# Optimization experiments

Hardware: AMD Instinct MI355X
Metric: run time of the kernel (lower is better)

Reference implementation:

```python
import jax, jax.numpy as jnp
import numpy as np

PATCH = 4
WINDOW = 4
MAX_ROUNDS = 4
MIN_ROUNDS = 2
LAMBDA_P = 0.2
TOPK = 8


def _ln(x, g, b, eps=1e-5):
    m = x.mean(-1, keepdims=True)
    v = ((x - m) ** 2).mean(-1, keepdims=True)
    return (x - m) / jnp.sqrt(v + eps) * g + b


def _mlp(x, w1, b1, w2, b2):
    # Linear -> exact GELU -> Linear (matches nn.GELU default)
    return jax.nn.gelu(x @ w1 + b1, approximate=False) @ w2 + b2


def setup_inputs() -> dict:
    key = jax.random.key(0)
    ks = jax.random.split(key, 24)
    B, T, D, V = 16, 4096, 256, 256
    s = 0.02
    w = lambda i, shape: jax.random.normal(ks[i], shape, jnp.float32) * s
    z = lambda *shape: jnp.zeros(shape, jnp.float32)
    o = lambda *shape: jnp.ones(shape, jnp.float32)
    return {
        'x': jax.random.randint(ks[0], (B, T), 0, V),
        'emb': w(1, (V, D)), 'pos': w(2, (PATCH, D)),
        'gru_wih': w(3, (D, 3 * D)), 'gru_whh': w(4, (D, 3 * D)),
        'gru_bih': z(3 * D), 'gru_bhh': z(3 * D),
        'ln_p_g': o(D), 'ln_p_b': z(D),
        'sum_w': w(5, (D, D)), 'sum_b': z(D),
        'msg_w1': w(6, (2 * D, D)), 'msg_b1': z(D), 'msg_w2': w(7, (D, D)), 'msg_b2': z(D),
        'upd_w1': w(8, (2 * D, D)), 'upd_b1': z(D), 'upd_w2': w(9, (D, D)), 'upd_b2': z(D),
        'halt_w': w(10, (D, 1)), 'halt_b': z(1),
        'ln_mp_g': o(D), 'ln_mp_b': z(D),
        'q_w': w(11, (D, D)), 'q_b': z(D),
        'k_w': w(12, (D, D)), 'k_b': z(D),
        'v_w': w(13, (D, D)), 'v_b': z(D),
        'o_w': w(14, (D, D)), 'o_b': z(D),
        'bc_w': w(15, (D, D)), 'bc_b': z(D),
        'ln_f_g': o(D), 'ln_f_b': z(D),
        'head_w': w(16, (D, V)),
    }


def reference(x, emb, pos, gru_wih, gru_whh, gru_bih, gru_bhh, ln_p_g, ln_p_b,
              sum_w, sum_b, msg_w1, msg_b1, msg_w2, msg_b2, upd_w1, upd_b1,
              upd_w2, upd_b2, halt_w, halt_b, ln_mp_g, ln_mp_b, q_w, q_b,
              k_w, k_b, v_w, v_b, o_w, o_b, bc_w, bc_b, ln_f_g, ln_f_b, head_w):
    B, T = x.shape
    D = emb.shape[1]
    Np = T // PATCH  # T is divisible by PATCH for these shapes (no pad needed)

    # --- GRU patch processor over B*Np sequences of length PATCH ---
    tok = x.reshape(B * Np, PATCH)
    hseq = emb[tok] + pos[None]  # [BN, P, D]

    def gru_step(h, xt):
        gi = xt @ gru_wih + gru_bih
        gh = h @ gru_whh + gru_bhh
        ir, iz, inn = jnp.split(gi, 3, -1)
        hr, hz, hn = jnp.split(gh, 3, -1)
        r = jax.nn.sigmoid(ir + hr)
        zz = jax.nn.sigmoid(iz + hz)
        n = jnp.tanh(inn + r * hn)
        h = (1 - zz) * n + zz * h
        return h, h

    h0 = jnp.zeros((B * Np, D), hseq.dtype)
    _, gout = jax.lax.scan(gru_step, h0, jnp.swapaxes(hseq, 0, 1))
    local = _ln(jnp.swapaxes(gout, 0, 1), ln_p_g, ln_p_b).reshape(B, Np, PATCH, D)
    summaries = local.mean(2) @ sum_w + sum_b  # [B, Np, D]

    # --- Local message passing with ACT-style halting (fixed MAX_ROUNDS) ---
    h = summaries
    remaining = jnp.ones((B, Np, 1), h.dtype)
    out_mp = jnp.zeros_like(h)
    kl = jnp.zeros((), h.dtype)
    for step in range(MAX_ROUNDS):
        padded = jnp.pad(h, ((0, 0), (WINDOW, 0), (0, 0)))
        # neighbors: self plus previous WINDOW patches -> [B, Np, W+1, D]
        neigh = jnp.stack([padded[:, WINDOW - w:WINDOW - w + Np] for w in range(WINDOW + 1)], axis=2)
        self_exp = jnp.broadcast_to(h[:, :, None, :], neigh.shape)
        msgs = _mlp(jnp.concatenate([self_exp, neigh], -1), msg_w1, msg_b1, msg_w2, msg_b2).mean(2)
        h = _ln(h + _mlp(jnp.concatenate([h, msgs], -1), upd_w1, upd_b1, upd_w2, upd_b2), ln_mp_g, ln_mp_b)
        if step < MIN_ROUNDS:
            hp = jnp.zeros((B, Np, 1), h.dtype)
        else:
            hp = jax.nn.sigmoid(h.mean(1, keepdims=True) @ halt_w + halt_b)  # [B,1,1]
            hp = jnp.broadcast_to(hp, (B, Np, 1))
        if step == MAX_ROUNDS - 1:
            hp = jnp.ones_like(hp)
        out_mp = out_mp + remaining * hp * h
        remaining = remaining * (1 - hp)
        p_geom = LAMBDA_P * (1 - LAMBDA_P) ** step
        # F.kl_div(log(mean+eps), log(p_geom), log_target=True) = p*(log p - log(mean+eps))
        kl = kl + p_geom * (np.log(p_geom) - jnp.log(hp.mean() + 1e-8))
    kl = kl / MAX_ROUNDS

    # --- Sparse top-k causal retrieval ---
    q = out_mp @ q_w + q_b
    kk = out_mp @ k_w + k_b
    v = out_mp @ v_w + v_b
    scores = jnp.einsum('bnd,bmd->bnm', q, kk) / np.sqrt(D).astype(np.float32)
    causal = jnp.tril(jnp.ones((Np, Np), bool))
    neg = jnp.asarray(-jnp.inf, scores.dtype)
    scores = jnp.where(causal[None], scores, neg)
    vals, idx = jax.lax.top_k(scores, TOPK)  # [B, Np, k]
    bi = jnp.arange(B)[:, None, None]
    ni = jnp.arange(Np)[None, :, None]
    sparse = jnp.full_like(scores, neg).at[bi, ni, idx].set(vals)
    attn = jax.nn.softmax(sparse, axis=-1)
    retrieved = jnp.einsum('bnm,bmd->bnd', attn, v) @ o_w + o_b

    # --- Broadcast back to tokens and project ---
    combined = out_mp + retrieved
    broad = combined @ bc_w + bc_b
    final = (local + broad[:, :, None, :]).reshape(B, Np * PATCH, D)[:, :T]
    logits = _ln(final, ln_f_g, ln_f_b) @ head_w
    return logits, kl
```

## Files before the change

### kernel.cpp

```cpp
#include <hip/hip_runtime.h>
#include <math.h>


typedef __bf16 bf16_t;
typedef bf16_t bf16x8 __attribute__((ext_vector_type(8)));
typedef bf16_t bf16x4 __attribute__((ext_vector_type(4)));
typedef float f32x4 __attribute__((ext_vector_type(4)));

#define GF_BIAS 1
#define GF_GELU 4
#define GF_RES 8
#define GF_SCAUSAL 16
#define GF_F32OUT 32

__device__ __forceinline__ float gelu_exact(float x) {
  return 0.5f * x * (1.0f + erff(x * 0.7071067811865475f));
}

__device__ __forceinline__ float sigm(float x) { return 1.f / (1.f + expf(-x)); }

__device__ __forceinline__ float wave_sum(float v) {
#pragma unroll
  for (int o = 32; o; o >>= 1) v += __shfl_xor(v, o, 64);
  return v;
}

__device__ __forceinline__ void gload16(const void* g, void* l) {
  __builtin_amdgcn_global_load_lds(
      (const __attribute__((address_space(1))) void*)g,
      (__attribute__((address_space(3))) void*)l, 16, 0, 0);
}

__device__ __forceinline__ unsigned long long skey(float s, int m) {
  unsigned u = __float_as_uint(s);
  u ^= (u & 0x80000000u) ? 0xFFFFFFFFu : 0x80000000u;
  return ((unsigned long long)u << 32) | (unsigned)(0x7FFFFFFF - m);
}

template<int FLAGS>
__global__ __launch_bounds__(256)
void gemm_bt(const bf16_t* __restrict__ A, const bf16_t* __restrict__ Bt,
             void* __restrict__ Cv, const float* __restrict__ bias,
             const bf16_t* __restrict__ res,
             int lda, int ldb, int ldc, int ldr,
             long long sA, long long sB, long long sC, float scale)
{
  __shared__ __align__(16) bf16_t As[128][64];
  __shared__ __align__(16) bf16_t Bs[128][64];
  const int z = blockIdx.z;
  A  += (long long)z * sA;
  Bt += (long long)z * sB;
  const int m0 = blockIdx.x * 128, n0 = blockIdx.y * 128;
  if ((FLAGS & GF_SCAUSAL) && n0 > m0) return;
  const int tid = threadIdx.x, lane = tid & 63, wave = tid >> 6;
  const int wm = (wave >> 1) << 6, wn = (wave & 1) << 6;
  const int lr = lane & 15, lg = lane >> 4;
  const int cx = lane & 7;

  const int srow = wave * 32 + (lane >> 3);
  const int scol = (((lane & 7) ^ ((lane >> 3) & 7)) * 8);
  const bf16_t* ga = A  + (long long)(m0 + srow) * lda + scol;
  const bf16_t* gb = Bt + (long long)(n0 + srow) * ldb + scol;
  char* lA = (char*)(&As[srow][0]) + (lane & 7) * 16;
  char* lB = (char*)(&Bs[srow][0]) + (lane & 7) * 16;

  f32x4 acc[4][4] = {};

#pragma unroll
  for (int kt = 0; kt < 4; kt++) {
    const int ko = kt * 64;
#pragma unroll
    for (int q = 0; q < 4; q++) {
      gload16(ga + (long long)q * 8 * lda + ko, lA + q * 1024);
      gload16(gb + (long long)q * 8 * ldb + ko, lB + q * 1024);
    }
    __syncthreads();
#pragma unroll
    for (int kk = 0; kk < 2; kk++) {
      const int co = ((kk * 4 + lg) ^ cx) << 4;
      bf16x8 af[4], bfv[4];
#pragma unroll
      for (int i = 0; i < 4; i++)
        af[i]  = *(const bf16x8*)((char*)As + (wm + i * 16 + lr) * 128 + co);
#pragma unroll
      for (int j = 0; j < 4; j++)
        bfv[j] = *(const bf16x8*)((char*)Bs + (wn + j * 16 + lr) * 128 + co);
#pragma unroll
      for (int i = 0; i < 4; i++)
#pragma unroll
        for (int j = 0; j < 4; j++)
          acc[i][j] = __builtin_amdgcn_mfma_f32_16x16x32_bf16(af[i], bfv[j], acc[i][j], 0, 0, 0);
    }
    if (kt < 3) __syncthreads();
  }

#pragma unroll
  for (int i = 0; i < 4; i++) {
#pragma unroll
    for (int j = 0; j < 4; j++) {
      const int col = n0 + wn + j * 16 + lr;
      const float bval = (FLAGS & GF_BIAS) ? bias[col] : 0.f;
#pragma unroll
      for (int e = 0; e < 4; e++) {
        const int row = m0 + wm + i * 16 + lg * 4 + e;
        float v = acc[i][j][e];
        if (FLAGS & GF_SCAUSAL) { v *= scale; if (col > row) v = -__builtin_inff(); }
        v += bval;
        if (FLAGS & GF_RES) v += (float)res[(long long)row * ldr + col];
        if (FLAGS & GF_GELU) v = gelu_exact(v);
        const long long ci = (long long)z * sC + (long long)row * ldc + col;
        if (FLAGS & GF_F32OUT) ((float*)Cv)[ci] = v;
        else                   ((bf16_t*)Cv)[ci] = (bf16_t)v;
      }
    }
  }
}

template<int FLAGS>
__global__ __launch_bounds__(256)
void gemm64(const bf16_t* __restrict__ A, const bf16_t* __restrict__ Bt,
            void* __restrict__ Cv, const float* __restrict__ bias,
            const bf16_t* __restrict__ res,
            int lda, int ldb, int ldc, int ldr)
{
  __shared__ __align__(16) bf16_t As[64][64];
  __shared__ __align__(16) bf16_t Bs[64][64];
  const int m0 = blockIdx.x * 64, n0 = blockIdx.y * 64;
  const int tid = threadIdx.x, lane = tid & 63, wave = tid >> 6;
  const int wm = (wave >> 1) * 32, wn = (wave & 1) * 32;
  const int lr = lane & 15, lg = lane >> 4;
  const int cx = lane & 7;

  const int srow = tid >> 3;
  const int scol = (((tid & 7) ^ (srow & 7)) * 8);
  const bf16_t* ga = A  + (long long)(m0 + srow) * lda + scol;
  const bf16_t* gb = Bt + (long long)(n0 + srow) * ldb + scol;
  char* lA = (char*)As + tid * 16;
  char* lB = (char*)Bs + tid * 16;

  f32x4 acc[2][2] = {};

#pragma unroll
  for (int kt = 0; kt < 4; kt++) {
    const int ko = kt * 64;
    gload16(ga + ko, lA);
    gload16(ga + 32LL * lda + ko, lA + 4096);
    gload16(gb + ko, lB);
    gload16(gb + 32LL * ldb + ko, lB + 4096);
    __syncthreads();
#pragma unroll
    for (int kk = 0; kk < 2; kk++) {
      const int co = ((kk * 4 + lg) ^ cx) << 4;
      bf16x8 af[2], bfv[2];
#pragma unroll
      for (int i = 0; i < 2; i++)
        af[i]  = *(const bf16x8*)((char*)As + (wm + i * 16 + lr) * 128 + co);
#pragma unroll
      for (int j = 0; j < 2; j++)
        bfv[j] = *(const bf16x8*)((char*)Bs + (wn + j * 16 + lr) * 128 + co);
#pragma unroll
      for (int i = 0; i < 2; i++)
#pragma unroll
        for (int j = 0; j < 2; j++)
          acc[i][j] = __builtin_amdgcn_mfma_f32_16x16x32_bf16(af[i], bfv[j], acc[i][j], 0, 0, 0);
    }
    if (kt < 3) __syncthreads();
  }

#pragma unroll
  for (int i = 0; i < 2; i++) {
#pragma unroll
    for (int j = 0; j < 2; j++) {
      const int col = n0 + wn + j * 16 + lr;
      const float bval = (FLAGS & GF_BIAS) ? bias[col] : 0.f;
#pragma unroll
      for (int e = 0; e < 4; e++) {
        const int row = m0 + wm + i * 16 + lg * 4 + e;
        float v = acc[i][j][e] + bval;
        if (FLAGS & GF_RES) v += (float)res[(long long)row * ldr + col];
        if (FLAGS & GF_GELU) v = gelu_exact(v);
        const long long ci = (long long)row * ldc + col;
        if (FLAGS & GF_F32OUT) ((float*)Cv)[ci] = v;
        else                   ((bf16_t*)Cv)[ci] = (bf16_t)v;
      }
    }
  }
}

struct TD { const float* src; bf16_t* dst; int N; int k0; int ld; };
struct PrepArgs {
  TD d[16];
  const float* emb; const float* pos; bf16_t* XE;
  const float* msg_b1; const float* msg_b2; const float* upd_w1; const float* upd_b1;
  const float* q_b; const float* k_b; const float* v_b;
  float* BIAS3; float* QKVB;
};

__global__ __launch_bounds__(256) void k_prep(PrepArgs pa) {
  const int y = blockIdx.y, x = blockIdx.x, d = threadIdx.x;
  if (y < 16) {
    TD t = pa.d[y];
    if (x >= t.N) return;
    if (t.k0 < 0) t.dst[(long long)x * 256 + d] = (bf16_t)t.src[(long long)x * t.ld + d];
    else          t.dst[(long long)x * 256 + d] = (bf16_t)t.src[(long long)(t.k0 + d) * t.ld + x];
  } else if (y == 16) {
    const int p = x >> 8, v = x & 255;
    pa.XE[(long long)x * 256 + d] = (bf16_t)(pa.emb[v * 256 + d] + pa.pos[p * 256 + d]);
  } else {
    if      (x == 0) pa.BIAS3[d] = pa.msg_b1[d];
    else if (x == 1) pa.BIAS3[256 + d] = 0.f;
    else if (x == 2) {
      float acc = pa.upd_b1[d];
      for (int k = 0; k < 256; k++) acc += pa.msg_b2[k] * pa.upd_w1[(long long)(256 + k) * 256 + d];
      pa.BIAS3[512 + d] = acc;
    }
    else if (x == 3) pa.QKVB[d] = pa.q_b[d];
    else if (x == 4) pa.QKVB[256 + d] = pa.k_b[d];
    else if (x == 5) pa.QKVB[512 + d] = pa.v_b[d];
  }
}

__global__ __launch_bounds__(64)
void k_gru_gate(const int* __restrict__ x, const bf16_t* __restrict__ gitab,
                const bf16_t* __restrict__ GH, const float* __restrict__ bhh,
                bf16_t* __restrict__ H, bf16_t* __restrict__ LOC, int t)
{
  const int s = blockIdx.x, lane = threadIdx.x, d0 = lane * 4;
  const int v = x[s * 4 + t];
  const bf16_t* gi = gitab + (long long)(t * 256 + v) * 768;
  const bf16x4 g_r = *(const bf16x4*)(gi + d0);
  const bf16x4 g_z = *(const bf16x4*)(gi + 256 + d0);
  const bf16x4 g_n = *(const bf16x4*)(gi + 512 + d0);
  float hr[4], hz[4], hn[4], hp[4];
  if (t == 0) {
#pragma unroll
    for (int e = 0; e < 4; e++) {
      hr[e] = bhh[d0 + e]; hz[e] = bhh[256 + d0 + e]; hn[e] = bhh[512 + d0 + e];
      hp[e] = 0.f;
    }
  } else {
    const bf16_t* gh = GH + (long long)s * 768;
    const bf16x4 a = *(const bf16x4*)(gh + d0);
    const bf16x4 b4 = *(const bf16x4*)(gh + 256 + d0);
    const bf16x4 c4 = *(const bf16x4*)(gh + 512 + d0);
    const bf16x4 hv = *(const bf16x4*)(H + (long long)s * 256 + d0);
#pragma unroll
    for (int e = 0; e < 4; e++) { hr[e] = a[e]; hz[e] = b4[e]; hn[e] = c4[e]; hp[e] = hv[e]; }
  }
  bf16x4 ho;
#pragma unroll
  for (int e = 0; e < 4; e++) {
    const float r = sigm((float)g_r[e] + hr[e]);
    const float zz = sigm((float)g_z[e] + hz[e]);
    const float nn = tanhf((float)g_n[e] + r * hn[e]);
    ho[e] = (bf16_t)((1.f - zz) * nn + zz * hp[e]);
  }
  *(bf16x4*)(H + (long long)s * 256 + d0) = ho;
  *(bf16x4*)(LOC + ((long long)s * 4 + t) * 256 + d0) = ho;
}

__global__ __launch_bounds__(64)
void k_ln(const bf16_t* __restrict__ X, const bf16_t* __restrict__ ADD, int addmode,
          bf16_t* __restrict__ OUT, const float* __restrict__ g,
          const float* __restrict__ b)
{
  const long long r = blockIdx.x;
  const int d0 = threadIdx.x * 4;
  const bf16x4 xv = *(const bf16x4*)(X + r * 256 + d0);
  float xf[4];
#pragma unroll
  for (int e = 0; e < 4; e++) xf[e] = (float)xv[e];
  if (addmode == 1) {
    const bf16x4 av = *(const bf16x4*)(ADD + r * 256 + d0);
#pragma unroll
    for (int e = 0; e < 4; e++) xf[e] += (float)av[e];
  } else if (addmode == 2) {
    const bf16x4 av = *(const bf16x4*)(ADD + (r >> 2) * 256 + d0);
#pragma unroll
    for (int e = 0; e < 4; e++) xf[e] += (float)av[e];
  }
  const float mean = wave_sum(xf[0] + xf[1] + xf[2] + xf[3]) * (1.f / 256.f);
  float q = 0.f;
#pragma unroll
  for (int e = 0; e < 4; e++) { const float dx = xf[e] - mean; q += dx * dx; }
  const float rstd = rsqrtf(wave_sum(q) * (1.f / 256.f) + 1e-5f);
  const float4 gv = *(const float4*)(g + d0);
  const float4 bv = *(const float4*)(b + d0);
  const float gg[4] = {gv.x, gv.y, gv.z, gv.w};
  const float bb[4] = {bv.x, bv.y, bv.z, bv.w};
  bf16x4 ov;
#pragma unroll
  for (int e = 0; e < 4; e++) ov[e] = (bf16_t)((xf[e] - mean) * rstd * gg[e] + bb[e]);
  *(bf16x4*)(OUT + r * 256 + d0) = ov;
}

__global__ __launch_bounds__(64)
void k_lnp4(bf16_t* __restrict__ LOC, bf16_t* __restrict__ SUMB,
            const float* __restrict__ g, const float* __restrict__ b)
{
  const long long s = blockIdx.x;
  const int d0 = threadIdx.x * 4;
  const float4 gv = *(const float4*)(g + d0);
  const float4 bv = *(const float4*)(b + d0);
  const float gg[4] = {gv.x, gv.y, gv.z, gv.w};
  const float bb[4] = {bv.x, bv.y, bv.z, bv.w};
  float accd[4] = {0.f, 0.f, 0.f, 0.f};
#pragma unroll
  for (int t = 0; t < 4; t++) {
    bf16_t* row = LOC + (s * 4 + t) * 256 + d0;
    const bf16x4 xv = *(const bf16x4*)row;
    float xf[4];
#pragma unroll
    for (int e = 0; e < 4; e++) xf[e] = (float)xv[e];
    const float mean = wave_sum(xf[0] + xf[1] + xf[2] + xf[3]) * (1.f / 256.f);
    float q = 0.f;
#pragma unroll
    for (int e = 0; e < 4; e++) { const float dx = xf[e] - mean; q += dx * dx; }
    const float rstd = rsqrtf(wave_sum(q) * (1.f / 256.f) + 1e-5f);
    bf16x4 ov;
#pragma unroll
    for (int e = 0; e < 4; e++) {
      const float y = (xf[e] - mean) * rstd * gg[e] + bb[e];
      ov[e] = (bf16_t)y;
      accd[e] += y;
    }
    *(bf16x4*)row = ov;
  }
  bf16x4 sv;
#pragma unroll
  for (int e = 0; e < 4; e++) sv[e] = (bf16_t)(accd[e] * 0.25f);
  *(bf16x4*)(SUMB + s * 256 + d0) = sv;
}

__global__ __launch_bounds__(64)
void k_gelumix(const bf16_t* __restrict__ A3, bf16_t* __restrict__ G)
{
  const long long s = blockIdx.x;
  const int n = (int)(s & 1023);
  const int d0 = threadIdx.x * 4;
  const bf16x4 av = *(const bf16x4*)(A3 + s * 768 + d0);
  float a[4];
#pragma unroll
  for (int e = 0; e < 4; e++) a[e] = (float)av[e];
  float acc[4] = {0.f, 0.f, 0.f, 0.f};
  const bf16_t* bbase = A3 + s * 768 + 256 + d0;
#pragma unroll
  for (int w = 0; w <= 4; w++) {
    if (n >= w) {
      const bf16x4 bn = *(const bf16x4*)(bbase - (long long)w * 768);
#pragma unroll
      for (int e = 0; e < 4; e++) acc[e] += gelu_exact(a[e] + (float)bn[e]);
    } else {
#pragma unroll
      for (int e = 0; e < 4; e++) acc[e] += gelu_exact(a[e]);
    }
  }
  bf16x4 ov;
#pragma unroll
  for (int e = 0; e < 4; e++) ov[e] = (bf16_t)(acc[e] * 0.2f);
  *(bf16x4*)(G + s * 256 + d0) = ov;
}

__global__ __launch_bounds__(64)
void k_halt1(const bf16_t* __restrict__ Hm, float* __restrict__ PS) {
  const int c = blockIdx.x, b = blockIdx.y, d0 = threadIdx.x * 4;
  float acc[4] = {0.f, 0.f, 0.f, 0.f};
  const bf16_t* base = Hm + ((long long)b * 1024 + c * 32) * 256 + d0;
#pragma unroll 4
  for (int n = 0; n < 32; n++) {
    const bf16x4 hv = *(const bf16x4*)(base + (long long)n * 256);
#pragma unroll
    for (int e = 0; e < 4; e++) acc[e] += (float)hv[e];
  }
  float4 o4; o4.x = acc[0]; o4.y = acc[1]; o4.z = acc[2]; o4.w = acc[3];
  *(float4*)(PS + ((long long)b * 32 + c) * 256 + d0) = o4;
}

__global__ __launch_bounds__(64)
void k_halt2(const float* __restrict__ PS, const float* __restrict__ hw,
             const float* __restrict__ hb, float* __restrict__ HP) {
  const int b = blockIdx.x, d0 = threadIdx.x * 4;
  float acc[4] = {0.f, 0.f, 0.f, 0.f};
  for (int c = 0; c < 32; c++) {
    const float4 p4 = *(const float4*)(PS + ((long long)b * 32 + c) * 256 + d0);
    acc[0] += p4.x; acc[1] += p4.y; acc[2] += p4.z; acc[3] += p4.w;
  }
  const float4 w4 = *(const float4*)(hw + d0);
  float val = (acc[0] * w4.x + acc[1] * w4.y + acc[2] * w4.z + acc[3] * w4.w) * (1.f / 1024.f);
  val = wave_sum(val);
  if (threadIdx.x == 0) HP[b] = sigm(val + hb[0]);
}

__global__ void k_kl(const float* __restrict__ HP, float* __restrict__ out) {
  float s = 0.f;
  for (int b = 0; b < 16; b++) s += HP[b];
  const float hpm = s * (1.f / 16.f);
  const float l8 = logf(1e-8f);
  const float p0 = 0.2f, p1 = 0.16f, p2 = 0.128f, p3 = 0.1024f;
  const float kl = p0 * (logf(p0) - l8)
                 + p1 * (logf(p1) - l8)
                 + p2 * (logf(p2) - logf(hpm + 1e-8f))
                 + p3 * (logf(p3) - logf(1.f + 1e-8f));
  out[0] = kl * 0.25f;
}

__global__ __launch_bounds__(64)
void k_outmp(const bf16_t* __restrict__ Hm, const float* __restrict__ HP,
             bf16_t* __restrict__ O, int acc) {
  const long long s = blockIdx.x;
  const int d0 = threadIdx.x * 4;
  const int b = (int)(s >> 10);
  const float hp = HP[b];
  const bf16x4 hv = *(const bf16x4*)(Hm + s * 256 + d0);
  bf16x4 ov;
  if (acc) {
    const bf16x4 pv = *(const bf16x4*)(O + s * 256 + d0);
#pragma unroll
    for (int e = 0; e < 4; e++) ov[e] = (bf16_t)((float)pv[e] + (1.f - hp) * (float)hv[e]);
  } else {
#pragma unroll
    for (int e = 0; e < 4; e++) ov[e] = (bf16_t)(hp * (float)hv[e]);
  }
  *(bf16x4*)(O + s * 256 + d0) = ov;
}

__global__ __launch_bounds__(256)
void k_topk(const float* __restrict__ S, const bf16_t* __restrict__ QKV,
            bf16_t* __restrict__ O) {
  const int n = blockIdx.x * 4 + (threadIdx.x >> 6);
  const int b = blockIdx.y;
  const int lane = threadIdx.x & 63;
  const float* srow = S + ((long long)(b * 1024 + n)) * 1024;
  unsigned long long kv[8] = {0, 0, 0, 0, 0, 0, 0, 0};
  for (int mb = lane * 4; mb <= n; mb += 256) {
    const float4 s4 = *(const float4*)(srow + mb);
    const float sv[4] = {s4.x, s4.y, s4.z, s4.w};
#pragma unroll
    for (int jj = 0; jj < 4; jj++) {
      const int m = mb + jj;
      if (m <= n) {
        const unsigned long long k = skey(sv[jj], m);
        if (k > kv[7]) {
          kv[7] = k;
#pragma unroll
          for (int j = 7; j > 0; j--) {
            if (kv[j] > kv[j-1]) {
              const unsigned long long t = kv[j]; kv[j] = kv[j-1]; kv[j-1] = t;
            }
          }
        }
      }
    }
  }
  float wv[8]; int wi[8];
#pragma unroll
  for (int r = 0; r < 8; r++) {
    unsigned long long mk = kv[0];
#pragma unroll
    for (int off = 32; off; off >>= 1) {
      const unsigned long long ok = __shfl_xor(mk, off, 64);
      if (ok > mk) mk = ok;
    }
    if (mk != 0ull) {
      unsigned hi = (unsigned)(mk >> 32);
      hi ^= (hi & 0x80000000u) ? 0x80000000u : 0xFFFFFFFFu;
      wv[r] = __uint_as_float(hi);
      wi[r] = 0x7FFFFFFF - (int)(unsigned)(mk & 0xFFFFFFFFu);
    } else {
      wv[r] = 0.f; wi[r] = -1;
    }
    if (kv[0] == mk && mk != 0ull) {
#pragma unroll
      for (int j = 0; j < 7; j++) kv[j] = kv[j + 1];
      kv[7] = 0ull;
    }
  }
  const float mx = wv[0];
  float w[8]; float den = 0.f;
#pragma unroll
  for (int j = 0; j < 8; j++) {
    w[j] = (wi[j] >= 0) ? expf(wv[j] - mx) : 0.f;
    den += w[j];
  }
  const float inv = 1.f / den;
  float a[4] = {0.f, 0.f, 0.f, 0.f};
#pragma unroll
  for (int j = 0; j < 8; j++) {
    if (wi[j] >= 0) {
      const bf16x4 vv = *(const bf16x4*)(QKV + ((long long)b * 1024 + wi[j]) * 768 + 512 + lane * 4);
      const float wj = w[j] * inv;
#pragma unroll
      for (int e = 0; e < 4; e++) a[e] = fmaf(wj, (float)vv[e], a[e]);
    }
  }
  bf16x4 o4;
#pragma unroll
  for (int e = 0; e < 4; e++) o4[e] = (bf16_t)a[e];
  *(bf16x4*)(O + ((long long)(b * 1024 + n)) * 256 + lane * 4) = o4;
}

extern "C" void kernel_launch(void* const* d_in, const int* in_sizes, int n_in,
                              void* d_out, int out_size, void* d_ws, size_t ws_size,
                              hipStream_t stream) {
  (void)in_sizes; (void)n_in; (void)ws_size;
  const int*   x      = (const int*)d_in[0];
  const float* emb    = (const float*)d_in[1];
  const float* pos    = (const float*)d_in[2];
  const float* wih    = (const float*)d_in[3];
  const float* whh    = (const float*)d_in[4];
  const float* bih    = (const float*)d_in[5];
  const float* bhh    = (const float*)d_in[6];
  const float* lnp_g  = (const float*)d_in[7];
  const float* lnp_b  = (const float*)d_in[8];
  const float* sum_w  = (const float*)d_in[9];
  const float* sum_b  = (const float*)d_in[10];
  const float* msg_w1 = (const float*)d_in[11];
  const float* msg_b1 = (const float*)d_in[12];
  const float* msg_w2 = (const float*)d_in[13];
  const float* msg_b2 = (const float*)d_in[14];
  const float* upd_w1 = (const float*)d_in[15];
  const float* upd_b1 = (const float*)d_in[16];
  const float* upd_w2 = (const float*)d_in[17];
  const float* upd_b2 = (const float*)d_in[18];
  const float* halt_w = (const float*)d_in[19];
  const float* halt_b = (const float*)d_in[20];
  const float* lnm_g  = (const float*)d_in[21];
  const float* lnm_b  = (const float*)d_in[22];
  const float* q_b    = (const float*)d_in[24];
  const float* k_b    = (const float*)d_in[26];
  const float* v_b    = (const float*)d_in[28];
  const float* o_b    = (const float*)d_in[30];
  const float* bc_b   = (const float*)d_in[32];
  const float* lnf_g  = (const float*)d_in[33];
  const float* lnf_b  = (const float*)d_in[34];

  char* base = (char*)d_ws;
  size_t off = 0;
  auto alloc = [&](size_t bytes) -> void* {
    void* p = (void*)(base + off);
    off += (bytes + 255) & ~(size_t)255;
    return p;
  };
  const size_t SL2 = 16384ull * 256 * 2;
  bf16_t* WIHT  = (bf16_t*)alloc(768 * 256 * 2);
  bf16_t* WHHT  = (bf16_t*)alloc(768 * 256 * 2);
  bf16_t* SUMT  = (bf16_t*)alloc(256 * 256 * 2);
  bf16_t* MW    = (bf16_t*)alloc(768 * 256 * 2);
  bf16_t* W2T   = (bf16_t*)alloc(256 * 256 * 2);
  bf16_t* W2NT  = (bf16_t*)alloc(256 * 256 * 2);
  bf16_t* UW1MT = (bf16_t*)alloc(256 * 256 * 2);
  bf16_t* UW2T  = (bf16_t*)alloc(256 * 256 * 2);
  bf16_t* WCB   = (bf16_t*)alloc(256 * 256 * 2);
  bf16_t* QKVW  = (bf16_t*)alloc(768 * 256 * 2);
  bf16_t* OT    = (bf16_t*)alloc(256 * 256 * 2);
  bf16_t* BCT   = (bf16_t*)alloc(256 * 256 * 2);
  bf16_t* HEADT = (bf16_t*)alloc(256 * 256 * 2);
  float*  BIAS3 = (float*)alloc(768 * 4);
  float*  QKVB  = (float*)alloc(768 * 4);
  bf16_t* XE    = (bf16_t*)alloc(1024ull * 256 * 2);
  bf16_t* GITAB = (bf16_t*)alloc(1024ull * 768 * 2);
  bf16_t* LOCb  = (bf16_t*)alloc(65536ull * 256 * 2);

  char*   SCR   = (char*)alloc(16ull * 1024 * 1024 * 4);
  float*  SCORES = (float*)SCR;
  bf16_t* GH    = (bf16_t*)SCR;
  bf16_t* H     = (bf16_t*)(SCR + 25165824);
  bf16_t* SUMB  = (bf16_t*)(SCR + 33554432);
  bf16_t* A3    = (bf16_t*)(SCR + 41943040);

  bf16_t* HMP   = (bf16_t*)alloc(SL2);
  bf16_t* G     = (bf16_t*)alloc(SL2);
  bf16_t* BROAD = (bf16_t*)alloc(SL2);
  bf16_t* UB    = (bf16_t*)alloc(SL2);
  bf16_t* U2B   = (bf16_t*)alloc(SL2);
  bf16_t* OUTMP = (bf16_t*)alloc(SL2);
  bf16_t* QKV   = (bf16_t*)alloc(16384ull * 768 * 2);
  float*  PS    = (float*)alloc(512ull * 256 * 4);
  float*  HP    = (float*)alloc(64);
  bf16_t* ATT   = UB;
  bf16_t* COMB  = U2B;
  float*  out   = (float*)d_out;
  float*  klout = out + (out_size - 1);

  PrepArgs pa;
  pa.d[0]  = { wih,                    WIHT,            768, 0,   768 };
  pa.d[1]  = { whh,                    WHHT,            768, 0,   768 };
  pa.d[2]  = { sum_w,                  SUMT,            256, 0,   256 };
  pa.d[3]  = { msg_w1,                 MW,              256, 0,   256 };
  pa.d[4]  = { msg_w1,                 MW + 256 * 256,  256, 256, 256 };
  pa.d[5]  = { upd_w1,                 MW + 512 * 256,  256, 0,   256 };
  pa.d[6]  = { msg_w2,                 W2T,             256, 0,   256 };
  pa.d[7]  = { upd_w1,                 UW1MT,           256, 256, 256 };
  pa.d[8]  = { upd_w2,                 UW2T,            256, 0,   256 };
  pa.d[9]  = { (const float*)d_in[23], QKVW,            256, 0,   256 };
  pa.d[10] = { (const float*)d_in[25], QKVW + 256*256,  256, 0,   256 };
  pa.d[11] = { (const float*)d_in[27], QKVW + 512*256,  256, 0,   256 };
  pa.d[12] = { (const float*)d_in[29], OT,              256, 0,   256 };
  pa.d[13] = { (const float*)d_in[31], BCT,             256, 0,   256 };
  pa.d[14] = { (const float*)d_in[35], HEADT,           256, 0,   256 };
  pa.d[15] = { msg_w2,                 W2NT,            256, -1,  256 };
  pa.emb = emb; pa.pos = pos; pa.XE = XE;
  pa.msg_b1 = msg_b1; pa.msg_b2 = msg_b2; pa.upd_w1 = upd_w1; pa.upd_b1 = upd_b1;
  pa.q_b = q_b; pa.k_b = k_b; pa.v_b = v_b;
  pa.BIAS3 = BIAS3; pa.QKVB = QKVB;
  k_prep<<<dim3(1024, 18), 256, 0, stream>>>(pa);

  gemm64<0><<<dim3(4, 4), 256, 0, stream>>>(
      UW1MT, W2NT, WCB, nullptr, nullptr, 256, 256, 256, 0);

  gemm64<GF_BIAS><<<dim3(16, 12), 256, 0, stream>>>(
      XE, WIHT, GITAB, bih, nullptr, 256, 256, 768, 0);

  k_gru_gate<<<16384, 64, 0, stream>>>(x, GITAB, GH, bhh, H, LOCb, 0);
  for (int t = 1; t < 4; t++) {
    gemm64<GF_BIAS><<<dim3(256, 12), 256, 0, stream>>>(
        H, WHHT, GH, bhh, nullptr, 256, 256, 768, 0);
    k_gru_gate<<<16384, 64, 0, stream>>>(x, GITAB, GH, bhh, H, LOCb, t);
  }

  k_lnp4<<<16384, 64, 0, stream>>>(LOCb, SUMB, lnp_g, lnp_b);
  gemm64<GF_BIAS><<<dim3(256, 4), 256, 0, stream>>>(
      SUMB, SUMT, HMP, sum_b, nullptr, 256, 256, 256, 0);

  for (int step = 0; step < 4; step++) {
    gemm64<GF_BIAS><<<dim3(256, 12), 256, 0, stream>>>(
        HMP, MW, A3, BIAS3, nullptr, 256, 256, 768, 0);
    k_gelumix<<<16384, 64, 0, stream>>>(A3, G);
    gemm64<GF_RES | GF_GELU><<<dim3(256, 4), 256, 0, stream>>>(
        G, WCB, UB, nullptr, A3 + 512, 256, 256, 256, 768);
    gemm64<GF_BIAS><<<dim3(256, 4), 256, 0, stream>>>(
        UB, UW2T, U2B, upd_b2, nullptr, 256, 256, 256, 0);
    k_ln<<<16384, 64, 0, stream>>>(HMP, U2B, 1, HMP, lnm_g, lnm_b);
    if (step == 2) {
      k_halt1<<<dim3(32, 16), 64, 0, stream>>>(HMP, PS);
      k_halt2<<<16, 64, 0, stream>>>(PS, halt_w, halt_b, HP);
      k_kl<<<1, 1, 0, stream>>>(HP, klout);
      k_outmp<<<16384, 64, 0, stream>>>(HMP, HP, OUTMP, 0);
    } else if (step == 3) {
      k_outmp<<<16384, 64, 0, stream>>>(HMP, HP, OUTMP, 1);
    }
  }

  gemm64<GF_BIAS><<<dim3(256, 12), 256, 0, stream>>>(
      OUTMP, QKVW, QKV, QKVB, nullptr, 256, 256, 768, 0);
  gemm_bt<GF_SCAUSAL | GF_F32OUT><<<dim3(8, 8, 16), 256, 0, stream>>>(
      QKV, QKV + 256, SCORES, nullptr, nullptr, 768, 768, 1024, 0,
      1024LL * 768, 1024LL * 768, 1024LL * 1024, 0.0625f);
  k_topk<<<dim3(256, 16), 256, 0, stream>>>(SCORES, QKV, ATT);
  gemm64<GF_BIAS | GF_RES><<<dim3(256, 4), 256, 0, stream>>>(
      ATT, OT, COMB, o_b, OUTMP, 256, 256, 256, 256);
  gemm64<GF_BIAS><<<dim3(256, 4), 256, 0, stream>>>(
      COMB, BCT, BROAD, bc_b, nullptr, 256, 256, 256, 0);

  k_ln<<<65536, 64, 0, stream>>>(LOCb, BROAD, 2, LOCb, lnf_g, lnf_b);
  gemm_bt<GF_F32OUT><<<dim3(512, 2, 1), 256, 0, stream>>>(
      LOCb, HEADT, out, nullptr, nullptr, 256, 256, 256, 0, 0, 0, 0, 1.f);
}
```

Measured before the change: 491.6 us.

## Fuse causal score GEMM with top-k retrieval; use 128-tile GEMM for N=768

Replaces the batched causal score GEMM plus separate top-k kernel with a single kernel. Each wave computes 16 query rows' scores against key tiles using MFMA, keeps a running top-8 per row, then applies softmax and gathers V. This avoids writing and re-reading the 64 MB fp32 score matrix. It also switches the three 768-wide projection GEMMs from 64x64 tiles to the 128x128 gemm_bt kernel. The fused kernel launches only 1024 single-wave blocks with causal work imbalance, so it may be latency bound.

```diff
diff --git a/kernel.cpp b/kernel.cpp
--- a/kernel.cpp
+++ b/kernel.cpp
@@ -10,7 +10,6 @@
 #define GF_BIAS 1
 #define GF_GELU 4
 #define GF_RES 8
-#define GF_SCAUSAL 16
 #define GF_F32OUT 32
 
 __device__ __forceinline__ float gelu_exact(float x) {
@@ -42,16 +41,11 @@
 void gemm_bt(const bf16_t* __restrict__ A, const bf16_t* __restrict__ Bt,
              void* __restrict__ Cv, const float* __restrict__ bias,
              const bf16_t* __restrict__ res,
-             int lda, int ldb, int ldc, int ldr,
-             long long sA, long long sB, long long sC, float scale)
+             int lda, int ldb, int ldc, int ldr)
 {
   __shared__ __align__(16) bf16_t As[128][64];
   __shared__ __align__(16) bf16_t Bs[128][64];
-  const int z = blockIdx.z;
-  A  += (long long)z * sA;
-  Bt += (long long)z * sB;
   const int m0 = blockIdx.x * 128, n0 = blockIdx.y * 128;
-  if ((FLAGS & GF_SCAUSAL) && n0 > m0) return;
   const int tid = threadIdx.x, lane = tid & 63, wave = tid >> 6;
   const int wm = (wave >> 1) << 6, wn = (wave & 1) << 6;
   const int lr = lane & 15, lg = lane >> 4;
@@ -103,12 +97,10 @@
 #pragma unroll
       for (int e = 0; e < 4; e++) {
         const int row = m0 + wm + i * 16 + lg * 4 + e;
-        float v = acc[i][j][e];
-        if (FLAGS & GF_SCAUSAL) { v *= scale; if (col > row) v = -__builtin_inff(); }
-        v += bval;
+        float v = acc[i][j][e] + bval;
         if (FLAGS & GF_RES) v += (float)res[(long long)row * ldr + col];
         if (FLAGS & GF_GELU) v = gelu_exact(v);
-        const long long ci = (long long)z * sC + (long long)row * ldc + col;
+        const long long ci = (long long)row * ldc + col;
         if (FLAGS & GF_F32OUT) ((float*)Cv)[ci] = v;
         else                   ((bf16_t*)Cv)[ci] = (bf16_t)v;
       }
@@ -184,6 +176,135 @@
         else                   ((bf16_t*)Cv)[ci] = (bf16_t)v;
       }
     }
+  }
+}
+
+__global__ __launch_bounds__(64)
+void k_fatopk(const bf16_t* __restrict__ QKV, bf16_t* __restrict__ O) {
+  const int b = blockIdx.y;
+  const int qw = (int)((blockIdx.x + ((blockIdx.y * 21) & 63)) & 63);
+  const int lane = threadIdx.x;
+  const int lr = lane & 15, lg = lane >> 4;
+  const bf16_t* Qp = QKV + (long long)b * (1024LL * 768);
+  const bf16_t* Kp = Qp + 256;
+  const bf16_t* Vp = Qp + 512;
+  const int q0 = qw * 16;
+  const int qrow = q0 + lr;
+
+  bf16x8 bq[8];
+#pragma unroll
+  for (int s = 0; s < 8; s++)
+    bq[s] = *(const bf16x8*)(Qp + (long long)qrow * 768 + s * 32 + lg * 8);
+
+  unsigned long long kv[8] = {0ull, 0ull, 0ull, 0ull, 0ull, 0ull, 0ull, 0ull};
+
+#define INS8(KEY) {                                                     \
+    const unsigned long long k_ = (KEY);                                \
+    if (k_ > kv[7]) {                                                   \
+      kv[7] = k_;                                                       \
+      _Pragma("unroll")                                                 \
+      for (int j_ = 7; j_ > 0; j_--)                                    \
+        if (kv[j_] > kv[j_-1]) {                                        \
+          const unsigned long long t_ = kv[j_];                         \
+          kv[j_] = kv[j_-1]; kv[j_-1] = t_;                             \
+        }                                                               \
+    }                                                                   \
+  }
+
+  const int klim = qw + 1;
+  for (int kt = 0; kt < klim; kt += 2) {
+    const int kt2 = (kt + 1 < klim) ? kt + 1 : kt;
+    const bf16_t* ka = Kp + (long long)(kt  * 16 + lr) * 768 + lg * 8;
+    const bf16_t* kb = Kp + (long long)(kt2 * 16 + lr) * 768 + lg * 8;
+    bf16x8 afA[8], afB[8];
+#pragma unroll
+    for (int s = 0; s < 8; s++) afA[s] = *(const bf16x8*)(ka + s * 32);
+#pragma unroll
+    for (int s = 0; s < 8; s++) afB[s] = *(const bf16x8*)(kb + s * 32);
+    f32x4 a0 = {}, a1 = {};
+#pragma unroll
+    for (int s = 0; s < 8; s += 2) {
+      a0 = __builtin_amdgcn_mfma_f32_16x16x32_bf16(afA[s],     bq[s],     a0, 0, 0, 0);
+      a1 = __builtin_amdgcn_mfma_f32_16x16x32_bf16(afA[s + 1], bq[s + 1], a1, 0, 0, 0);
+    }
+#pragma unroll
+    for (int e = 0; e < 4; e++) {
+      const int m = kt * 16 + lg * 4 + e;
+      if (m <= qrow) INS8(skey((a0[e] + a1[e]) * 0.0625f, m));
+    }
+    if (kt2 != kt) {
+      f32x4 b0 = {}, b1 = {};
+#pragma unroll
+      for (int s = 0; s < 8; s += 2) {
+        b0 = __builtin_amdgcn_mfma_f32_16x16x32_bf16(afB[s],     bq[s],     b0, 0, 0, 0);
+        b1 = __builtin_amdgcn_mfma_f32_16x16x32_bf16(afB[s + 1], bq[s + 1], b1, 0, 0, 0);
+      }
+#pragma unroll
+      for (int e = 0; e < 4; e++) {
+        const int m = kt2 * 16 + lg * 4 + e;
+        if (m <= qrow) INS8(skey((b0[e] + b1[e]) * 0.0625f, m));
+      }
+    }
+  }
+#undef INS8
+
+  float wv[8]; int wi[8];
+#pragma unroll
+  for (int r = 0; r < 8; r++) {
+    unsigned long long mk = kv[0];
+    unsigned long long ok = __shfl_xor(mk, 16, 64); if (ok > mk) mk = ok;
+    ok = __shfl_xor(mk, 32, 64); if (ok > mk) mk = ok;
+    if (mk != 0ull) {
+      unsigned hi = (unsigned)(mk >> 32);
+      hi ^= (hi & 0x80000000u) ? 0x80000000u : 0xFFFFFFFFu;
+      wv[r] = __uint_as_float(hi);
+      wi[r] = 0x7FFFFFFF - (int)(unsigned)(mk & 0xFFFFFFFFu);
+    } else {
+      wv[r] = 0.f; wi[r] = -1;
+    }
+    if (kv[0] == mk && mk != 0ull) {
+#pragma unroll
+      for (int j = 0; j < 7; j++) kv[j] = kv[j + 1];
+      kv[7] = 0ull;
+    }
+  }
+
+  const float mx = wv[0];
+  float w8[8]; float den = 0.f;
+#pragma unroll
+  for (int j = 0; j < 8; j++) {
+    w8[j] = (wi[j] >= 0) ? expf(wv[j] - mx) : 0.f;
+    den += w8[j];
+  }
+  const float inv = 1.f / den;
+
+  f32x4 av[16] = {};
+#pragma unroll
+  for (int j = 0; j < 8; j++) {
+    if (wi[j] >= 0) {
+      const float wj = w8[j] * inv;
+      const bf16_t* vr = Vp + (long long)wi[j] * 768 + lg * 64;
+#pragma unroll
+      for (int c = 0; c < 8; c++) {
+        const bf16x8 vv = *(const bf16x8*)(vr + c * 8);
+#pragma unroll
+        for (int e = 0; e < 4; e++) {
+          av[2 * c][e]     = fmaf(wj, (float)vv[e],     av[2 * c][e]);
+          av[2 * c + 1][e] = fmaf(wj, (float)vv[4 + e], av[2 * c + 1][e]);
+        }
+      }
+    }
+  }
+  bf16_t* op = O + ((long long)b * 1024 + qrow) * 256 + lg * 64;
+#pragma unroll
+  for (int c = 0; c < 8; c++) {
+    bf16x8 ov;
+#pragma unroll
+    for (int e = 0; e < 4; e++) {
+      ov[e]     = (bf16_t)av[2 * c][e];
+      ov[4 + e] = (bf16_t)av[2 * c + 1][e];
+    }
+    *(bf16x8*)(op + c * 8) = ov;
   }
 }
 
@@ -422,81 +543,6 @@
     for (int e = 0; e < 4; e++) ov[e] = (bf16_t)(hp * (float)hv[e]);
   }
   *(bf16x4*)(O + s * 256 + d0) = ov;
-}
-
-__global__ __launch_bounds__(256)
-void k_topk(const float* __restrict__ S, const bf16_t* __restrict__ QKV,
-            bf16_t* __restrict__ O) {
-  const int n = blockIdx.x * 4 + (threadIdx.x >> 6);
-  const int b = blockIdx.y;
-  const int lane = threadIdx.x & 63;
-  const float* srow = S + ((long long)(b * 1024 + n)) * 1024;
-  unsigned long long kv[8] = {0, 0, 0, 0, 0, 0, 0, 0};
-  for (int mb = lane * 4; mb <= n; mb += 256) {
-    const float4 s4 = *(const float4*)(srow + mb);
-    const float sv[4] = {s4.x, s4.y, s4.z, s4.w};
-#pragma unroll
-    for (int jj = 0; jj < 4; jj++) {
-      const int m = mb + jj;
-      if (m <= n) {
-        const unsigned long long k = skey(sv[jj], m);
-        if (k > kv[7]) {
-          kv[7] = k;
-#pragma unroll
-          for (int j = 7; j > 0; j--) {
-            if (kv[j] > kv[j-1]) {
-              const unsigned long long t = kv[j]; kv[j] = kv[j-1]; kv[j-1] = t;
-            }
-          }
-        }
-      }
-    }
-  }
-  float wv[8]; int wi[8];
-#pragma unroll
-  for (int r = 0; r < 8; r++) {
-    unsigned long long mk = kv[0];
-#pragma unroll
-    for (int off = 32; off; off >>= 1) {
-      const unsigned long long ok = __shfl_xor(mk, off, 64);
-      if (ok > mk) mk = ok;
-    }
-    if (mk != 0ull) {
-      unsigned hi = (unsigned)(mk >> 32);
-      hi ^= (hi & 0x80000000u) ? 0x80000000u : 0xFFFFFFFFu;
-      wv[r] = __uint_as_float(hi);
-      wi[r] = 0x7FFFFFFF - (int)(unsigned)(mk & 0xFFFFFFFFu);
-    } else {
-      wv[r] = 0.f; wi[r] = -1;
-    }
-    if (kv[0] == mk && mk != 0ull) {
-#pragma unroll
-      for (int j = 0; j < 7; j++) kv[j] = kv[j + 1];
-      kv[7] = 0ull;
-    }
-  }
-  const float mx = wv[0];
-  float w[8]; float den = 0.f;
-#pragma unroll
-  for (int j = 0; j < 8; j++) {
-    w[j] = (wi[j] >= 0) ? expf(wv[j] - mx) : 0.f;
-    den += w[j];
-  }
-  const float inv = 1.f / den;
-  float a[4] = {0.f, 0.f, 0.f, 0.f};
-#pragma unroll
-  for (int j = 0; j < 8; j++) {
-    if (wi[j] >= 0) {
-      const bf16x4 vv = *(const bf16x4*)(QKV + ((long long)b * 1024 + wi[j]) * 768 + 512 + lane * 4);
-      const float wj = w[j] * inv;
-#pragma unroll
-      for (int e = 0; e < 4; e++) a[e] = fmaf(wj, (float)vv[e], a[e]);
-    }
-  }
-  bf16x4 o4;
-#pragma unroll
-  for (int e = 0; e < 4; e++) o4[e] = (bf16_t)a[e];
-  *(bf16x4*)(O + ((long long)(b * 1024 + n)) * 256 + lane * 4) = o4;
 }
 
 extern "C" void kernel_launch(void* const* d_in, const int* in_sizes, int n_in,
@@ -562,7 +608,6 @@
   bf16_t* LOCb  = (bf16_t*)alloc(65536ull * 256 * 2);
 
   char*   SCR   = (char*)alloc(16ull * 1024 * 1024 * 4);
-  float*  SCORES = (float*)SCR;
   bf16_t* GH    = (bf16_t*)SCR;
   bf16_t* H     = (bf16_t*)(SCR + 25165824);
   bf16_t* SUMB  = (bf16_t*)(SCR + 33554432);
@@ -613,7 +658,7 @@
 
   k_gru_gate<<<16384, 64, 0, stream>>>(x, GITAB, GH, bhh, H, LOCb, 0);
   for (int t = 1; t < 4; t++) {
-    gemm64<GF_BIAS><<<dim3(256, 12), 256, 0, stream>>>(
+    gemm_bt<GF_BIAS><<<dim3(128, 6), 256, 0, stream>>>(
         H, WHHT, GH, bhh, nullptr, 256, 256, 768, 0);
     k_gru_gate<<<16384, 64, 0, stream>>>(x, GITAB, GH, bhh, H, LOCb, t);
   }
@@ -623,7 +668,7 @@
       SUMB, SUMT, HMP, sum_b, nullptr, 256, 256, 256, 0);
 
   for (int step = 0; step < 4; step++) {
-    gemm64<GF_BIAS><<<dim3(256, 12), 256, 0, stream>>>(
+    gemm_bt<GF_BIAS><<<dim3(128, 6), 256, 0, stream>>>(
         HMP, MW, A3, BIAS3, nullptr, 256, 256, 768, 0);
     k_gelumix<<<16384, 64, 0, stream>>>(A3, G);
     gemm64<GF_RES | GF_GELU><<<dim3(256, 4), 256, 0, stream>>>(
@@ -641,18 +686,15 @@
     }
   }
 
-  gemm64<GF_BIAS><<<dim3(256, 12), 256, 0, stream>>>(
+  gemm_bt<GF_BIAS><<<dim3(128, 6), 256, 0, stream>>>(
       OUTMP, QKVW, QKV, QKVB, nullptr, 256, 256, 768, 0);
-  gemm_bt<GF_SCAUSAL | GF_F32OUT><<<dim3(8, 8, 16), 256, 0, stream>>>(
-      QKV, QKV + 256, SCORES, nullptr, nullptr, 768, 768, 1024, 0,
-      1024LL * 768, 1024LL * 768, 1024LL * 1024, 0.0625f);
-  k_topk<<<dim3(256, 16), 256, 0, stream>>>(SCORES, QKV, ATT);
+  k_fatopk<<<dim3(64, 16), 64, 0, stream>>>(QKV, ATT);
   gemm64<GF_BIAS | GF_RES><<<dim3(256, 4), 256, 0, stream>>>(
       ATT, OT, COMB, o_b, OUTMP, 256, 256, 256, 256);
   gemm64<GF_BIAS><<<dim3(256, 4), 256, 0, stream>>>(
       COMB, BCT, BROAD, bc_b, nullptr, 256, 256, 256, 0);
 
   k_ln<<<65536, 64, 0, stream>>>(LOCb, BROAD, 2, LOCb, lnf_g, lnf_b);
-  gemm_bt<GF_F32OUT><<<dim3(512, 2, 1), 256, 0, stream>>>(
-      LOCb, HEADT, out, nullptr, nullptr, 256, 256, 256, 0, 0, 0, 0, 1.f);
-}
+  gemm_bt<GF_F32OUT><<<dim3(512, 2), 256, 0, stream>>>(
+      LOCb, HEADT, out, nullptr, nullptr, 256, 256, 256, 0);
+}
```

New measurement: 487.5 us. No clear change (-0.8%).
